# Optimization experiments

Hardware: AMD Instinct MI355X
Metric: run time of the kernel (lower is better)

Reference implementation:

```python
import jax, jax.numpy as jnp
import numpy as np

_W1 = np.array([[[-1, 0, 0], [0, 1, 0], [0, 0, 0]],
                [[0, -1, 0], [0, 1, 0], [0, 0, 0]],
                [[0, 0, -1], [0, 1, 0], [0, 0, 0]],
                [[0, 0, 0], [-1, 1, 0], [0, 0, 0]]], dtype=np.float32).reshape(4, 1, 3, 3)
_W2 = _W1[:, :, ::-1, ::-1].copy()

BN_EPS = 1e-3  # YOLOX BaseConv BatchNorm eps
SHIFTS = (1, 3)


def _conv1x1(x, w, b=None):
    # x: (B,C,H,W), w: (O,C,1,1)
    y = jnp.einsum('bchw,oc->bohw', x, w[:, :, 0, 0])
    if b is not None:
        y = y + b[None, :, None, None]
    return y


def _grouped_dilated(x, w, d, groups):
    # 3x3 grouped conv, dilation d, 'same' padding (pad = d for 3x3)
    return jax.lax.conv_general_dilated(
        x, w, window_strides=(1, 1), padding=((d, d), (d, d)),
        rhs_dilation=(d, d), dimension_numbers=('NCHW', 'OIHW', 'NCHW'),
        feature_group_count=groups)


def setup_inputs() -> dict:
    key = jax.random.key(0)
    ks = jax.random.split(key, 6)
    B, C, H, W = 4, 128, 384, 384
    Cq = C // 4
    return {
        'cen': jax.random.normal(ks[0], (B, C, H, W), jnp.float32),
        'mas': jax.random.normal(ks[1], (B, 1, H, W), jnp.float32),
        'scales': jnp.zeros((4,), jnp.float32),
        'in_conv_w': jax.random.normal(ks[2], (Cq, C, 1, 1), jnp.float32) * 0.05,
        'in_conv_b': jnp.zeros((Cq,), jnp.float32),
        'base_w': jax.random.normal(ks[3], (Cq, Cq, 1, 1), jnp.float32) * 0.1,
        'bn_gamma': jnp.ones((Cq,), jnp.float32),
        'bn_beta': jnp.zeros((Cq,), jnp.float32),
        'bn_mean': jnp.zeros((Cq,), jnp.float32),
        'bn_var': jnp.ones((Cq,), jnp.float32),
        'out_w': jax.random.normal(ks[4], (1, Cq, 1, 1), jnp.float32) * 0.1,
        'out_b': jnp.zeros((1,), jnp.float32),
    }


def reference(cen, mas, scales, in_conv_w, in_conv_b, base_w,
              bn_gamma, bn_beta, bn_mean, bn_var, out_w, out_b):
    B, C, H, W = cen.shape
    Cq = C // 4
    k1 = jnp.asarray(np.tile(_W1, (Cq, 1, 1, 1)))  # (4*Cq,1,3,3)
    k2 = jnp.asarray(np.tile(_W2, (Cq, 1, 1, 1)))

    x = _conv1x1(cen, in_conv_w, in_conv_b)  # (B,Cq,H,W)
    outs = []
    for shift in SHIFTS:
        o1 = _grouped_dilated(x, k1, shift, Cq)  # (B,4*Cq,H,W)
        o2 = _grouped_dilated(x, k2, shift, Cq)
        o = (o1 * o2).reshape(B, Cq, 4, H, W).min(axis=2)
        outs.append(o)
    outs = jnp.stack(outs, axis=-1)  # (B,Cq,H,W,n_shifts)
    feat = jax.nn.relu(outs.max(axis=-1) + outs.mean(axis=-1))

    # out_conv = BaseConv(1x1, BN, SiLU) + Conv2d(Cq->1, 1x1)
    y = _conv1x1(feat, base_w)
    inv = jax.lax.rsqrt(bn_var + BN_EPS)
    y = (y - bn_mean[None, :, None, None]) * (bn_gamma * inv)[None, :, None, None] + bn_beta[None, :, None, None]
    y = jax.nn.silu(y)
    att = jax.nn.sigmoid(_conv1x1(y, out_w, out_b))  # (B,1,H,W)

    s = jax.nn.softmax(scales)
    m = jax.nn.sigmoid(mas)
    return cen * (att * m * s[0] + m * s[1] + s[2] * att + s[3])
```

## Files before the change

### kernel.cpp

```cpp
#include <hip/hip_runtime.h>

#define HH 384
#define WW 384
#define HWSZ (HH*WW)
#define CIN 128
#define CQ 32
#define NB 4
#define NPIX (NB*HWSZ)

__device__ __forceinline__ float sigmoidf_(float v){ return 1.0f/(1.0f + __expf(-v)); }

__global__ __launch_bounds__(256) void k_prep(
    const float* __restrict__ in_w, const float* __restrict__ base_w,
    const float* __restrict__ bn_g, const float* __restrict__ bn_b,
    const float* __restrict__ bn_m, const float* __restrict__ bn_v,
    const float* __restrict__ out_w, const float* __restrict__ out_b,
    const float* __restrict__ scales,
    float* __restrict__ wt, float* __restrict__ bt, float* __restrict__ prm){
  int t = threadIdx.x;
  for (int i = t; i < CIN*CQ; i += 256){ int c = i >> 5, o = i & 31; wt[i] = in_w[o*CIN + c]; }
  for (int i = t; i < CQ*CQ;  i += 256){ int c = i >> 5, o = i & 31; bt[i] = base_w[o*CQ + c]; }
  if (t < CQ){
    float inv = rsqrtf(bn_v[t] + 1e-3f);
    float g = bn_g[t]*inv;
    prm[t]      = g;
    prm[32 + t] = bn_b[t] - bn_m[t]*g;
    prm[64 + t] = out_w[t];
  }
  if (t == 0){
    float s0=scales[0], s1=scales[1], s2=scales[2], s3=scales[3];
    float mx = fmaxf(fmaxf(s0,s1), fmaxf(s2,s3));
    float e0=expf(s0-mx), e1=expf(s1-mx), e2=expf(s2-mx), e3=expf(s3-mx);
    float inv = 1.0f/(e0+e1+e2+e3);
    prm[96]=e0*inv; prm[97]=e1*inv; prm[98]=e2*inv; prm[99]=e3*inv;
    prm[100]=out_b[0];
  }
}

__global__ __launch_bounds__(256) void k_conv1(const float* __restrict__ cen,
    const float* __restrict__ wt, const float* __restrict__ bvec,
    float* __restrict__ x) {
  int t = threadIdx.x;
  int p0  = blockIdx.x * 512 + t*2;
  int b   = p0 / HWSZ;
  int pix = p0 - b*HWSZ;
  const float* cb = cen + (size_t)b*CIN*HWSZ + pix;
  float2 acc[CQ];
  #pragma unroll
  for (int o=0;o<CQ;o++){ float bb = bvec[o]; acc[o].x=bb; acc[o].y=bb; }

  float2 cur[4], nxt[4];
  #pragma unroll
  for (int k=0;k<4;k++) cur[k] = *(const float2*)(cb + (size_t)k*HWSZ);

  for (int c=0;c<CIN;c+=4){
    if (c+4 < CIN){
      #pragma unroll
      for (int k=0;k<4;k++) nxt[k] = *(const float2*)(cb + (size_t)(c+4+k)*HWSZ);
    }
    const float* wc = wt + c*CQ;
    #pragma unroll
    for (int k=0;k<4;k++){
      #pragma unroll
      for (int o=0;o<CQ;o++){
        float w = wc[k*CQ+o];
        acc[o].x = fmaf(cur[k].x, w, acc[o].x);
        acc[o].y = fmaf(cur[k].y, w, acc[o].y);
      }
    }
    #pragma unroll
    for (int k=0;k<4;k++) cur[k] = nxt[k];
  }
  float* xb = x + (size_t)b*CQ*HWSZ + pix;
  #pragma unroll
  for (int o=0;o<CQ;o++) *(float2*)(xb + (size_t)o*HWSZ) = acc[o];
}

#define TH 8
#define TW 64
#define LDSW 72
#define LDSN (14*LDSW)
#define GBX 6
#define GBY 48

__global__ __launch_bounds__(256) void k_att(const float* __restrict__ x,
    const float* __restrict__ mas, const float* __restrict__ bt,
    const float* __restrict__ prm, float* __restrict__ a_out) {
  __shared__ float tile[2][LDSN];
  int t = threadIdx.x;

  int gid = blockIdx.x;
  int b   = gid / (GBX*GBY);
  int rem = gid - b*(GBX*GBY);
  int ty  = rem / GBX;
  int tx  = rem - ty*GBX;
  int h0  = ty*TH, w0 = tx*TW;

  int soff[4]; float sval[4];
  #pragma unroll
  for (int j=0;j<4;j++){
    int i = t + j*256;
    int r = i / LDSW, cc = i - r*LDSW;
    int hh = h0 - 3 + r, wq = w0 - 3 + cc;
    bool ok = (i < LDSN) && (cc < 70) &&
              ((unsigned)hh < (unsigned)HH) && ((unsigned)wq < (unsigned)WW);
    soff[j] = ok ? (hh*WW + wq) : 0;
    sval[j] = ok ? 1.0f : 0.0f;
  }

  int rr = t >> 5;
  int ct = t & 31;
  const int R = 3 + rr, C = 3 + 2*ct;
  const int o_m3 = (R-3)*LDSW + C, o_m1 = (R-1)*LDSW + C,
            o_0  =  R   *LDSW + C, o_p1 = (R+1)*LDSW + C,
            o_p3 = (R+3)*LDSW + C;
  const float* xb = x + (size_t)b*CQ*HWSZ;

  float y0[CQ], y1[CQ];
  #pragma unroll
  for (int o=0;o<CQ;o++){ y0[o]=0.f; y1[o]=0.f; }

  float rg[4];
  #pragma unroll
  for (int j=0;j<4;j++) rg[j] = xb[soff[j]];

  #pragma unroll 2
  for (int c=0;c<CQ;c++){
    float* buf = tile[c&1];
    #pragma unroll
    for (int j=0;j<4;j++){
      int i = t + j*256;
      if (i < LDSN) buf[i] = sval[j]*rg[j];
    }
    float rg2[4];
    if (c+1 < CQ){
      const float* xn = xb + (size_t)(c+1)*HWSZ;
      #pragma unroll
      for (int j=0;j<4;j++) rg2[j] = xn[soff[j]];
    }
    __syncthreads();
    const float* p = buf;
    float2 m3a = *(const float2*)(p + o_m3 - 3);
    float  m3b0 = p[o_m3], m3b1 = p[o_m3 + 1];
    float2 m3c = *(const float2*)(p + o_m3 + 3);
    float2 m1a = *(const float2*)(p + o_m1 - 1);
    float2 m1b = *(const float2*)(p + o_m1 + 1);
    float2 z0  = *(const float2*)(p + o_0  - 3);
    float2 z1  = *(const float2*)(p + o_0  - 1);
    float2 z2  = *(const float2*)(p + o_0  + 1);
    float2 z3  = *(const float2*)(p + o_0  + 3);
    float2 p1a = *(const float2*)(p + o_p1 - 1);
    float2 p1b = *(const float2*)(p + o_p1 + 1);
    float2 p3a = *(const float2*)(p + o_p3 - 3);
    float  p3b0 = p[o_p3], p3b1 = p[o_p3 + 1];
    float2 p3c = *(const float2*)(p + o_p3 + 3);

    float xv = z1.y;
    float q0 = (xv-m1a.x)*(xv-p1b.x);
    float q1 = (xv-m1a.y)*(xv-p1a.y);
    float q2 = (xv-m1b.x)*(xv-p1a.x);
    float q3 = (xv-z1.x )*(xv-z2.x );
    float os0 = fminf(fminf(q0,q1),fminf(q2,q3));
    float r0 = (xv-m3a.x)*(xv-p3c.x);
    float r1 = (xv-m3b0 )*(xv-p3b0 );
    float r2 = (xv-m3c.x)*(xv-p3a.x);
    float r3 = (xv-z0.x )*(xv-z3.x );
    float os1 = fminf(fminf(r0,r1),fminf(r2,r3));
    float v0 = fmaxf(os0,os1) + 0.5f*(os0+os1);
    float fc0 = fmaxf(v0, 0.0f);

    float xw = z2.x;
    float u0 = (xw-m1a.y)*(xw-p1b.y);
    float u1 = (xw-m1b.x)*(xw-p1b.x);
    float u2 = (xw-m1b.y)*(xw-p1a.y);
    float u3 = (xw-z1.y )*(xw-z2.y );
    float ps0 = fminf(fminf(u0,u1),fminf(u2,u3));
    float s0 = (xw-m3a.y)*(xw-p3c.y);
    float s1 = (xw-m3b1 )*(xw-p3b1 );
    float s2 = (xw-m3c.y)*(xw-p3a.y);
    float s3 = (xw-z0.y )*(xw-z3.y );
    float ps1 = fminf(fminf(s0,s1),fminf(s2,s3));
    float v1 = fmaxf(ps0,ps1) + 0.5f*(ps0+ps1);
    float fc1 = fmaxf(v1, 0.0f);

    const float* wc = bt + c*CQ;
    #pragma unroll
    for (int o=0;o<CQ;o++){
      float w = wc[o];
      y0[o] = fmaf(fc0, w, y0[o]);
      y1[o] = fmaf(fc1, w, y1[o]);
    }
    #pragma unroll
    for (int j=0;j<4;j++) rg[j] = rg2[j];
  }

  float w0p=prm[96], w1p=prm[97], w2p=prm[98], w3p=prm[99], ob=prm[100];
  float lin0=ob, lin1=ob;
  #pragma unroll
  for (int o=0;o<CQ;o++){
    float g=prm[o], sh=prm[32+o], ow=prm[64+o];
    float yy0 = fmaf(y0[o], g, sh);
    float yy1 = fmaf(y1[o], g, sh);
    lin0 = fmaf(ow*yy0, sigmoidf_(yy0), lin0);
    lin1 = fmaf(ow*yy1, sigmoidf_(yy1), lin1);
  }
  float att0 = sigmoidf_(lin0);
  float att1 = sigmoidf_(lin1);

  int pa = b*HWSZ + (h0+rr)*WW + (w0 + 2*ct);
  float2 mm = *(const float2*)(mas + pa);
  float m0 = sigmoidf_(mm.x);
  float m1 = sigmoidf_(mm.y);
  float2 res;
  res.x = (att0*m0)*w0p + m0*w1p + att0*w2p + w3p;
  res.y = (att1*m1)*w0p + m1*w1p + att1*w2p + w3p;
  *(float2*)(a_out + pa) = res;
}

__global__ __launch_bounds__(256) void k_out(const float* __restrict__ cen,
    const float* __restrict__ a, float* __restrict__ out){
  unsigned i = blockIdx.x*256u + threadIdx.x;
  unsigned e = i*4u;
  unsigned bc  = e / HWSZ;
  unsigned pix = e - bc*HWSZ;
  unsigned b   = bc >> 7;
  float4 v  = ((const float4*)cen)[i];
  float4 av = ((const float4*)a)[(b*HWSZ + pix) >> 2];
  float4 r;
  r.x = v.x*av.x; r.y = v.y*av.y; r.z = v.z*av.z; r.w = v.w*av.w;
  ((float4*)out)[i] = r;
}

extern "C" void kernel_launch(void* const* d_in, const int* in_sizes, int n_in,
                              void* d_out, int out_size, void* d_ws, size_t ws_size,
                              hipStream_t stream) {
  const float* cen    = (const float*)d_in[0];
  const float* mas    = (const float*)d_in[1];
  const float* scales = (const float*)d_in[2];
  const float* in_w   = (const float*)d_in[3];
  const float* in_b   = (const float*)d_in[4];
  const float* base_w = (const float*)d_in[5];
  const float* bn_g   = (const float*)d_in[6];
  const float* bn_b   = (const float*)d_in[7];
  const float* bn_m   = (const float*)d_in[8];
  const float* bn_v   = (const float*)d_in[9];
  const float* out_w  = (const float*)d_in[10];
  const float* out_b  = (const float*)d_in[11];
  float* out = (float*)d_out;

  float* x   = (float*)d_ws;
  float* a   = x  + (size_t)NB*CQ*HWSZ;
  float* wt  = a  + (size_t)NB*HWSZ;
  float* bt  = wt + (size_t)CIN*CQ;
  float* prm = bt + (size_t)CQ*CQ;

  k_prep <<<1, 256, 0, stream>>>(in_w, base_w, bn_g, bn_b, bn_m, bn_v,
                                 out_w, out_b, scales, wt, bt, prm);
  k_conv1<<<NPIX/512, 256, 0, stream>>>(cen, wt, in_b, x);
  k_att  <<<NB*GBX*GBY, 256, 0, stream>>>(x, mas, bt, prm, a);
  k_out  <<<(NB*CIN*HWSZ)/1024, 256, 0, stream>>>(cen, a, out);
}
```

Before: 633.9 us.

## Fuse final channel scaling into attention kernel and use nontemporal cen loads

Removes the separate k_out kernel and the attention-map workspace. The attention kernel now multiplies all 128 channels of cen by its per-pixel factor and writes the output directly, with nontemporal loads and stores. conv1 also reads cen with nontemporal loads. This saves a launch and the write and reread of the attention map, but the att kernel's tail becomes a long memory loop, and its 8x64 tile rows give only short strided float2 accesses.

```diff
diff --git a/kernel.cpp b/kernel.cpp
--- a/kernel.cpp
+++ b/kernel.cpp
@@ -7,6 +7,8 @@
 #define CQ 32
 #define NB 4
 #define NPIX (NB*HWSZ)
+
+typedef float __attribute__((ext_vector_type(2))) f2v;
 
 __device__ __forceinline__ float sigmoidf_(float v){ return 1.0f/(1.0f + __expf(-v)); }
 
@@ -49,14 +51,14 @@
   #pragma unroll
   for (int o=0;o<CQ;o++){ float bb = bvec[o]; acc[o].x=bb; acc[o].y=bb; }
 
-  float2 cur[4], nxt[4];
-  #pragma unroll
-  for (int k=0;k<4;k++) cur[k] = *(const float2*)(cb + (size_t)k*HWSZ);
+  f2v cur[4], nxt[4];
+  #pragma unroll
+  for (int k=0;k<4;k++) cur[k] = __builtin_nontemporal_load((const f2v*)(cb + (size_t)k*HWSZ));
 
   for (int c=0;c<CIN;c+=4){
     if (c+4 < CIN){
       #pragma unroll
-      for (int k=0;k<4;k++) nxt[k] = *(const float2*)(cb + (size_t)(c+4+k)*HWSZ);
+      for (int k=0;k<4;k++) nxt[k] = __builtin_nontemporal_load((const f2v*)(cb + (size_t)(c+4+k)*HWSZ));
     }
     const float* wc = wt + c*CQ;
     #pragma unroll
@@ -84,8 +86,9 @@
 #define GBY 48
 
 __global__ __launch_bounds__(256) void k_att(const float* __restrict__ x,
-    const float* __restrict__ mas, const float* __restrict__ bt,
-    const float* __restrict__ prm, float* __restrict__ a_out) {
+    const float* __restrict__ cen, const float* __restrict__ mas,
+    const float* __restrict__ bt, const float* __restrict__ prm,
+    float* __restrict__ out) {
   __shared__ float tile[2][LDSN];
   int t = threadIdx.x;
 
@@ -207,28 +210,21 @@
   float att0 = sigmoidf_(lin0);
   float att1 = sigmoidf_(lin1);
 
-  int pa = b*HWSZ + (h0+rr)*WW + (w0 + 2*ct);
-  float2 mm = *(const float2*)(mas + pa);
+  int pix = (h0+rr)*WW + (w0 + 2*ct);
+  float2 mm = *(const float2*)(mas + b*HWSZ + pix);
   float m0 = sigmoidf_(mm.x);
   float m1 = sigmoidf_(mm.y);
-  float2 res;
-  res.x = (att0*m0)*w0p + m0*w1p + att0*w2p + w3p;
-  res.y = (att1*m1)*w0p + m1*w1p + att1*w2p + w3p;
-  *(float2*)(a_out + pa) = res;
-}
-
-__global__ __launch_bounds__(256) void k_out(const float* __restrict__ cen,
-    const float* __restrict__ a, float* __restrict__ out){
-  unsigned i = blockIdx.x*256u + threadIdx.x;
-  unsigned e = i*4u;
-  unsigned bc  = e / HWSZ;
-  unsigned pix = e - bc*HWSZ;
-  unsigned b   = bc >> 7;
-  float4 v  = ((const float4*)cen)[i];
-  float4 av = ((const float4*)a)[(b*HWSZ + pix) >> 2];
-  float4 r;
-  r.x = v.x*av.x; r.y = v.y*av.y; r.z = v.z*av.z; r.w = v.w*av.w;
-  ((float4*)out)[i] = r;
+  float a0 = (att0*m0)*w0p + m0*w1p + att0*w2p + w3p;
+  float a1 = (att1*m1)*w0p + m1*w1p + att1*w2p + w3p;
+
+  const float* cb = cen + (size_t)b*CIN*HWSZ + pix;
+  float*       od = out + (size_t)b*CIN*HWSZ + pix;
+  #pragma unroll 8
+  for (int c=0;c<CIN;c++){
+    f2v v = __builtin_nontemporal_load((const f2v*)(cb + (size_t)c*HWSZ));
+    v.x *= a0; v.y *= a1;
+    __builtin_nontemporal_store(v, (f2v*)(od + (size_t)c*HWSZ));
+  }
 }
 
 extern "C" void kernel_launch(void* const* d_in, const int* in_sizes, int n_in,
@@ -249,14 +245,12 @@
   float* out = (float*)d_out;
 
   float* x   = (float*)d_ws;
-  float* a   = x  + (size_t)NB*CQ*HWSZ;
-  float* wt  = a  + (size_t)NB*HWSZ;
+  float* wt  = x  + (size_t)NB*CQ*HWSZ;
   float* bt  = wt + (size_t)CIN*CQ;
   float* prm = bt + (size_t)CQ*CQ;
 
   k_prep <<<1, 256, 0, stream>>>(in_w, base_w, bn_g, bn_b, bn_m, bn_v,
                                  out_w, out_b, scales, wt, bt, prm);
   k_conv1<<<NPIX/512, 256, 0, stream>>>(cen, wt, in_b, x);
-  k_att  <<<NB*GBX*GBY, 256, 0, stream>>>(x, mas, bt, prm, a);
-  k_out  <<<(NB*CIN*HWSZ)/1024, 256, 0, stream>>>(cen, a, out);
-}
+  k_att  <<<NB*GBX*GBY, 256, 0, stream>>>(x, cen, mas, bt, prm, out);
+}
```

Measured after the change: 605.9 us. -4.4%, faster.
